# Kernel tuning notes

Measured on AMD Instinct MI355X. Metric: run time of the kernel, lower is better.

Reference implementation:

```python
import jax, jax.numpy as jnp
import numpy as np

EPS_COS = 1e-8
EPS_NORM = 1e-12
LN_EPS = 1e-5
OT_REG = 0.05
OT_ITERS = 5

B, L, D_IN, D_H = 16, 512, 1024, 1024


def setup_inputs() -> dict:
    key = jax.random.key(0)
    ks = jax.random.split(key, 16)
    p = lambda k, shape: 0.02 * jax.random.normal(k, shape, dtype=jnp.float32)
    return {
        "origin_seq": jax.random.normal(ks[0], (B, L, D_IN), dtype=jnp.float32),
        "target_seq": jax.random.normal(ks[1], (B, L, D_IN), dtype=jnp.float32),
        "W_ori": p(ks[2], (D_IN, D_H)), "b_ori": jnp.zeros((D_H,), jnp.float32),
        "W_tar": p(ks[3], (D_IN, D_H)), "b_tar": jnp.zeros((D_H,), jnp.float32),
        "W_ft": p(ks[4], (D_H, D_H)), "b_ft": jnp.zeros((D_H,), jnp.float32),
        "W_fo": p(ks[5], (D_H, D_H)), "b_fo": jnp.zeros((D_H,), jnp.float32),
        "W_fot": p(ks[6], (D_H, D_H)), "b_fot": jnp.zeros((D_H,), jnp.float32),
        "ln_g": jnp.ones((D_H,), jnp.float32), "ln_b": jnp.zeros((D_H,), jnp.float32),
    }


def _l2norm(x, eps):
    return x / jnp.maximum(jnp.linalg.norm(x, axis=-1, keepdims=True), eps)


def _forward(origin_seq, target_seq, W_ori, b_ori, W_tar, b_tar, W_ft, b_ft,
             W_fo, b_fo, W_fot, b_fot, ln_g, ln_b):
    ori = origin_seq @ W_ori + b_ori            # [B, Lo, H]
    tar = target_seq @ W_tar + b_tar            # [B, Lt, H]
    tar = tar @ W_ft + b_ft
    ori_fc = ori @ W_fo + b_fo
    ori_tp = ori @ W_fot + b_fot
    # cosine similarity cost: [B, Lt, Lo]
    C = jnp.einsum('bth,boh->bto', _l2norm(tar, EPS_COS), _l2norm(ori_fc, EPS_COS))
    # Sinkhorn: alternating row/col normalization of exp(C/eps)
    Q = jnp.exp(C / OT_REG)
    for _ in range(OT_ITERS):
        Q = Q / jnp.sum(Q, axis=-1, keepdims=True)
        Q = Q / jnp.sum(Q, axis=-2, keepdims=True)
    plan = _l2norm(Q, EPS_NORM)                 # F.normalize(dim=-1); dropout is eval no-op
    out = jnp.einsum('bto,boh->bth', plan, ori_tp) + tar
    mu = jnp.mean(out, axis=-1, keepdims=True)
    var = jnp.mean((out - mu) ** 2, axis=-1, keepdims=True)
    return ((out - mu) * jax.lax.rsqrt(var + LN_EPS)) * ln_g + ln_b


def reference(origin_seq, target_seq, W_ori, b_ori, W_tar, b_tar, W_ft, b_ft,
              W_fo, b_fo, W_fot, b_fot, ln_g, ln_b):
    return _forward(origin_seq, target_seq, W_ori, b_ori, W_tar, b_tar, W_ft, b_ft,
                    W_fo, b_fo, W_fot, b_fot, ln_g, ln_b)
```

## Files before the change

### kernel.cpp

```cpp
#include <hip/hip_runtime.h>
#include <hip/hip_bf16.h>
#include <math.h>

constexpr int Bn = 16;
constexpr int Ln = 512;
constexpr int Hn = 1024;
constexpr int RowsT = Bn * Ln;

typedef __attribute__((ext_vector_type(8))) short bf16x8;
typedef __attribute__((ext_vector_type(4))) float f32x4;
typedef __attribute__((ext_vector_type(8))) unsigned short u16x8;

__device__ __forceinline__ unsigned short f2bf(float f) {
  unsigned u = __float_as_uint(f);
  u += 0x7FFFu + ((u >> 16) & 1u);
  return (unsigned short)(u >> 16);
}
__device__ __forceinline__ float bf2f(unsigned short u) {
  return __uint_as_float(((unsigned)u) << 16);
}

__device__ __forceinline__ void gload_lds16(const void* g, void* l) {
  __builtin_amdgcn_global_load_lds(
      (const __attribute__((address_space(1))) void*)g,
      (__attribute__((address_space(3))) void*)l, 16, 0, 0);
}

__device__ __forceinline__ float block_reduce_sum(float v) {
  __shared__ float sbuf[8];
  const int lane = threadIdx.x & 63;
  const int wid = threadIdx.x >> 6;
#pragma unroll
  for (int off = 32; off > 0; off >>= 1) v += __shfl_down(v, off, 64);
  __syncthreads();
  if (lane == 0) sbuf[wid] = v;
  __syncthreads();
  if (threadIdx.x == 0) {
    float t = 0.f;
    const int nw = (blockDim.x + 63) >> 6;
    for (int i = 0; i < nw; ++i) t += sbuf[i];
    sbuf[0] = t;
  }
  __syncthreads();
  return sbuf[0];
}

__global__ __launch_bounds__(256) void conv_z(
    const float* __restrict__ s0, const float* __restrict__ s1,
    unsigned short* __restrict__ d0, unsigned short* __restrict__ d1) {
  const float* in = blockIdx.z ? s1 : s0;
  unsigned short* out = blockIdx.z ? d1 : d0;
  const size_t i = ((size_t)blockIdx.x * blockDim.x + threadIdx.x) * 8;
  const float4 a = *(const float4*)(in + i);
  const float4 b = *(const float4*)(in + i + 4);
  u16x8 r;
  r[0] = f2bf(a.x); r[1] = f2bf(a.y); r[2] = f2bf(a.z); r[3] = f2bf(a.w);
  r[4] = f2bf(b.x); r[5] = f2bf(b.y); r[6] = f2bf(b.z); r[7] = f2bf(b.w);
  *(u16x8*)(out + i) = r;
}

__global__ __launch_bounds__(256) void transpose_w3(
    const float* __restrict__ s0, const float* __restrict__ s1, const float* __restrict__ s2,
    unsigned short* __restrict__ d0, unsigned short* __restrict__ d1,
    unsigned short* __restrict__ d2, int K, int N) {
  const int z = blockIdx.z;
  const float* W = z == 0 ? s0 : (z == 1 ? s1 : s2);
  unsigned short* Wt = z == 0 ? d0 : (z == 1 ? d1 : d2);
  __shared__ float t[32][33];
  const int n0 = blockIdx.x * 32;
  const int k0 = blockIdx.y * 32;
  const int tx = threadIdx.x & 31;
  const int ty = threadIdx.x >> 5;
#pragma unroll
  for (int i = 0; i < 32; i += 8)
    t[ty + i][tx] = W[(size_t)(k0 + ty + i) * N + n0 + tx];
  __syncthreads();
#pragma unroll
  for (int i = 0; i < 32; i += 8)
    Wt[(size_t)(n0 + ty + i) * K + k0 + tx] = f2bf(t[tx][ty + i]);
}

__global__ __launch_bounds__(256) void bias_combine(
    const float* __restrict__ b1a, const float* __restrict__ Wa, const float* __restrict__ b2a,
    const float* __restrict__ b1b, const float* __restrict__ Wb, const float* __restrict__ b2b,
    const float* __restrict__ b1c, const float* __restrict__ Wc, const float* __restrict__ b2c,
    float* __restrict__ o0, float* __restrict__ o1, float* __restrict__ o2) {
  const int z = blockIdx.y;
  const float* b1 = z == 0 ? b1a : (z == 1 ? b1b : b1c);
  const float* W  = z == 0 ? Wa  : (z == 1 ? Wb  : Wc);
  const float* b2 = z == 0 ? b2a : (z == 1 ? b2b : b2c);
  float* out      = z == 0 ? o0  : (z == 1 ? o1  : o2);
  const int n = blockIdx.x * 256 + threadIdx.x;
  float s = b2[n];
  for (int j = 0; j < Hn; ++j) s += b1[j] * W[(size_t)j * Hn + n];
  out[n] = s;
}

#define MFMA_PROLOG(Aptr, Bptr, Kdim)                                          \
  constexpr int BK = 32;                                                       \
  __shared__ unsigned short As[128][BK];                                       \
  __shared__ unsigned short Bs[128][BK];                                       \
  const int tid = threadIdx.x;                                                 \
  const int wid = tid >> 6;                                                    \
  const int lane = tid & 63;                                                   \
  const int wr = (wid >> 1) * 64;                                              \
  const int wc = (wid & 1) * 64;                                               \
  const int sr = lane >> 2;                                                    \
  const int sk = (lane & 3) * 8;                                               \
  const size_t arow = (size_t)(row0 + wid * 32 + sr) * Kdim + sk;              \
  const size_t brow = (size_t)(col0 + wid * 32 + sr) * Kdim + sk;              \
  f32x4 acc[4][4] = {};                                                        \
  for (int k0 = 0; k0 < Kdim; k0 += BK) {                                      \
    gload_lds16(Aptr + arow + k0,                      &As[wid * 32][0]);      \
    gload_lds16(Aptr + arow + (size_t)16 * Kdim + k0,  &As[wid * 32 + 16][0]); \
    gload_lds16(Bptr + brow + k0,                      &Bs[wid * 32][0]);      \
    gload_lds16(Bptr + brow + (size_t)16 * Kdim + k0,  &Bs[wid * 32 + 16][0]); \
    __syncthreads();                                                           \
    bf16x8 af[4], bfr[4];                                                      \
    _Pragma("unroll")                                                          \
    for (int m = 0; m < 4; ++m)                                                \
      af[m] = *(const bf16x8*)&As[wr + m * 16 + (lane & 15)][(lane >> 4) * 8]; \
    _Pragma("unroll")                                                          \
    for (int n = 0; n < 4; ++n)                                                \
      bfr[n] = *(const bf16x8*)&Bs[wc + n * 16 + (lane & 15)][(lane >> 4) * 8];\
    _Pragma("unroll")                                                          \
    for (int m = 0; m < 4; ++m)                                                \
      _Pragma("unroll")                                                        \
      for (int n = 0; n < 4; ++n)                                              \
        acc[m][n] = __builtin_amdgcn_mfma_f32_16x16x32_bf16(af[m], bfr[n],     \
                                                            acc[m][n], 0, 0, 0);\
    __syncthreads();                                                           \
  }                                                                            \
  const int cr = (lane >> 4) * 4;                                              \
  const int cc = lane & 15;

__global__ __launch_bounds__(256) void mfma_gemm_w3(
    const unsigned short* __restrict__ A0, const unsigned short* __restrict__ A1,
    const unsigned short* __restrict__ A2,
    const unsigned short* __restrict__ B0, const unsigned short* __restrict__ B1,
    const unsigned short* __restrict__ B2,
    unsigned short* __restrict__ D0, unsigned short* __restrict__ D1,
    unsigned short* __restrict__ D2, int N, int K) {
  const int z = blockIdx.z;
  const unsigned short* A = z == 0 ? A0 : (z == 1 ? A1 : A2);
  const unsigned short* Bt = z == 0 ? B0 : (z == 1 ? B1 : B2);
  unsigned short* D = z == 0 ? D0 : (z == 1 ? D1 : D2);
  const int row0 = blockIdx.y * 128;
  const int col0 = blockIdx.x * 128;
  MFMA_PROLOG(A, Bt, K)
#pragma unroll
  for (int m = 0; m < 4; ++m) {
#pragma unroll
    for (int n = 0; n < 4; ++n) {
      const int gc = col0 + wc + n * 16 + cc;
#pragma unroll
      for (int r = 0; r < 4; ++r) {
        const int gr = row0 + wr + m * 16 + cr + r;
        D[(size_t)gr * N + gc] = f2bf(acc[m][n][r]);
      }
    }
  }
}

__global__ __launch_bounds__(256) void mfma_gemm_big(
    const unsigned short* __restrict__ Tb, const unsigned short* __restrict__ Ob,
    const unsigned short* __restrict__ W1, const unsigned short* __restrict__ W2,
    const unsigned short* __restrict__ W3,
    const float* __restrict__ bc1, const float* __restrict__ bc2,
    const float* __restrict__ bc3,
    unsigned short* __restrict__ Dtar, unsigned short* __restrict__ Dfc,
    unsigned short* __restrict__ DtpT) {
  const int id = blockIdx.x;
  const int xcd = id & 7;
  const int j = id >> 3;
  const int x = j & 7;
  const int rest = j >> 3;
  const int y = xcd + ((rest & 7) << 3);
  const int z = rest >> 3;
  const unsigned short* A = z == 0 ? Tb : Ob;
  const unsigned short* Bt = z == 0 ? W1 : (z == 1 ? W2 : W3);
  const float* bias = z == 0 ? bc1 : (z == 1 ? bc2 : bc3);
  const int row0 = y * 128;
  const int col0 = x * 128;
  MFMA_PROLOG(A, Bt, Hn)
  if (z != 2) {
    unsigned short* D = z == 0 ? Dtar : Dfc;
#pragma unroll
    for (int m = 0; m < 4; ++m) {
#pragma unroll
      for (int n = 0; n < 4; ++n) {
        const int gc = col0 + wc + n * 16 + cc;
        const float bv = bias[gc];
#pragma unroll
        for (int r = 0; r < 4; ++r) {
          const int gr = row0 + wr + m * 16 + cr + r;
          D[(size_t)gr * Hn + gc] = f2bf(acc[m][n][r] + bv);
        }
      }
    }
  } else {
#pragma unroll
    for (int m = 0; m < 4; ++m) {
      const int gr0 = row0 + wr + m * 16 + cr;
      const int b = gr0 >> 9;
      const int o = gr0 & 511;
#pragma unroll
      for (int n = 0; n < 4; ++n) {
        const int gc = col0 + wc + n * 16 + cc;
        const float bv = bias[gc];
        ushort4 w;
        w.x = f2bf(acc[m][n][0] + bv);
        w.y = f2bf(acc[m][n][1] + bv);
        w.z = f2bf(acc[m][n][2] + bv);
        w.w = f2bf(acc[m][n][3] + bv);
        *(ushort4*)(DtpT + ((size_t)b * Hn + gc) * Ln + o) = w;
      }
    }
  }
}

__global__ __launch_bounds__(256) void mfma_cos_exp(
    const unsigned short* __restrict__ TarBf, const unsigned short* __restrict__ FcBf,
    const float* __restrict__ rt, const float* __restrict__ rf,
    float* __restrict__ Q) {
  const int b = blockIdx.z;
  const unsigned short* Ab = TarBf + (size_t)b * Ln * Hn;
  const unsigned short* Bb = FcBf + (size_t)b * Ln * Hn;
  float* Qb = Q + (size_t)b * Ln * Ln;
  const int row0 = blockIdx.y * 128;
  const int col0 = blockIdx.x * 128;
  MFMA_PROLOG(Ab, Bb, Hn)
#pragma unroll
  for (int m = 0; m < 4; ++m) {
#pragma unroll
    for (int n = 0; n < 4; ++n) {
      const int o = col0 + wc + n * 16 + cc;
      const float rfo = rf[b * Ln + o] * 20.0f;
#pragma unroll
      for (int r = 0; r < 4; ++r) {
        const int t = row0 + wr + m * 16 + cr + r;
        const float c = acc[m][n][r] * rt[b * Ln + t] * rfo;
        Qb[(size_t)t * Ln + o] = __expf(c);
      }
    }
  }
}

__global__ __launch_bounds__(256) void mfma_out(
    const unsigned short* __restrict__ Plan, const unsigned short* __restrict__ TpT,
    const unsigned short* __restrict__ TarBf, float* __restrict__ Out) {
  const int b = blockIdx.z;
  const unsigned short* Ab = Plan + (size_t)b * Ln * Ln;
  const unsigned short* Bb = TpT + (size_t)b * Hn * Ln;
  const int row0 = blockIdx.y * 128;
  const int col0 = blockIdx.x * 128;
  MFMA_PROLOG(Ab, Bb, Ln)
#pragma unroll
  for (int m = 0; m < 4; ++m) {
#pragma unroll
    for (int n = 0; n < 4; ++n) {
      const int h = col0 + wc + n * 16 + cc;
#pragma unroll
      for (int r = 0; r < 4; ++r) {
        const int t = row0 + wr + m * 16 + cr + r;
        const size_t off = ((size_t)b * Ln + t) * Hn + h;
        Out[off] = acc[m][n][r] + bf2f(TarBf[off]);
      }
    }
  }
}

__global__ __launch_bounds__(256) void rownorm_z(
    const unsigned short* __restrict__ X0, const unsigned short* __restrict__ X1,
    float* __restrict__ r0, float* __restrict__ r1, float eps) {
  const unsigned short* X = blockIdx.y ? X1 : X0;
  float* r = blockIdx.y ? r1 : r0;
  const unsigned short* row = X + (size_t)blockIdx.x * Hn;
  const int i = threadIdx.x * 4;
  ushort4 v = *(const ushort4*)(row + i);
  float a0 = bf2f(v.x), a1 = bf2f(v.y), a2 = bf2f(v.z), a3 = bf2f(v.w);
  float s = block_reduce_sum(a0 * a0 + a1 * a1 + a2 * a2 + a3 * a3);
  if (threadIdx.x == 0) r[blockIdx.x] = 1.0f / fmaxf(sqrtf(s), eps);
}

__global__ __launch_bounds__(1024) void sinkhorn_fused(
    const float* __restrict__ Q, unsigned short* __restrict__ P) {
  const int b = blockIdx.x;
  const float* Qb = Q + (size_t)b * Ln * Ln;
  __shared__ __align__(16) float vsh[Ln];
  __shared__ __align__(16) float ush[Ln];
  __shared__ float part[1024];
  const int tid = threadIdx.x;
  const int wv = tid >> 6;
  const int lane = tid & 63;
  const int o = tid & 511;
  const int half = tid >> 9;
  if (tid < Ln) vsh[tid] = 1.0f;
  __syncthreads();
  for (int it = 0; it < 5; ++it) {
    for (int r = wv; r < Ln; r += 16) {
      const float* q = Qb + (size_t)r * Ln;
      const float4 a = *(const float4*)(q + lane * 8);
      const float4 c = *(const float4*)(q + lane * 8 + 4);
      const float4 va = *(const float4*)(vsh + lane * 8);
      const float4 vc = *(const float4*)(vsh + lane * 8 + 4);
      float s = a.x * va.x + a.y * va.y + a.z * va.z + a.w * va.w +
                c.x * vc.x + c.y * vc.y + c.z * vc.z + c.w * vc.w;
#pragma unroll
      for (int off = 32; off > 0; off >>= 1) s += __shfl_down(s, off, 64);
      if (lane == 0) ush[r] = 1.0f / s;
    }
    __syncthreads();
    float s = 0.f;
    const int t0 = half * 256;
#pragma unroll 4
    for (int t = t0; t < t0 + 256; ++t) s += Qb[(size_t)t * Ln + o] * ush[t];
    part[tid] = s;
    __syncthreads();
    if (tid < Ln) vsh[tid] = 1.0f / (part[tid] + part[tid + 512]);
    __syncthreads();
  }
  for (int r = wv; r < Ln; r += 16) {
    const float* q = Qb + (size_t)r * Ln;
    const float4 a = *(const float4*)(q + lane * 8);
    const float4 c = *(const float4*)(q + lane * 8 + 4);
    const float4 va = *(const float4*)(vsh + lane * 8);
    const float4 vc = *(const float4*)(vsh + lane * 8 + 4);
    float p[8];
    p[0] = a.x * va.x; p[1] = a.y * va.y; p[2] = a.z * va.z; p[3] = a.w * va.w;
    p[4] = c.x * vc.x; p[5] = c.y * vc.y; p[6] = c.z * vc.z; p[7] = c.w * vc.w;
    float s = 0.f;
#pragma unroll
    for (int k = 0; k < 8; ++k) s += p[k] * p[k];
#pragma unroll
    for (int off = 32; off > 0; off >>= 1) s += __shfl_down(s, off, 64);
    s = __shfl(s, 0, 64);
    const float rn = 1.0f / fmaxf(sqrtf(s), 1e-12f);
    u16x8 w;
#pragma unroll
    for (int k = 0; k < 8; ++k) w[k] = f2bf(p[k] * rn);
    *(u16x8*)(P + ((size_t)b * Ln + r) * Ln + lane * 8) = w;
  }
}

__global__ __launch_bounds__(256) void ln_kernel(
    float* __restrict__ Out, const float* __restrict__ g, const float* __restrict__ b) {
  float* row = Out + (size_t)blockIdx.x * Hn;
  const int tid = threadIdx.x;
  float4 v = reinterpret_cast<float4*>(row)[tid];
  float s = v.x + v.y + v.z + v.w;
  float ss = v.x * v.x + v.y * v.y + v.z * v.z + v.w * v.w;
  const float tot = block_reduce_sum(s);
  const float tot2 = block_reduce_sum(ss);
  const float mu = tot * (1.0f / Hn);
  const float var = tot2 * (1.0f / Hn) - mu * mu;
  const float rs = rsqrtf(var + 1e-5f);
  const float4 gg = reinterpret_cast<const float4*>(g)[tid];
  const float4 bb = reinterpret_cast<const float4*>(b)[tid];
  v.x = (v.x - mu) * rs * gg.x + bb.x;
  v.y = (v.y - mu) * rs * gg.y + bb.y;
  v.z = (v.z - mu) * rs * gg.z + bb.z;
  v.w = (v.w - mu) * rs * gg.w + bb.w;
  reinterpret_cast<float4*>(row)[tid] = v;
}

extern "C" void kernel_launch(void* const* d_in, const int* in_sizes, int n_in,
                              void* d_out, int out_size, void* d_ws, size_t ws_size,
                              hipStream_t stream) {
  const float* origin = (const float*)d_in[0];
  const float* target = (const float*)d_in[1];
  const float* W_ori = (const float*)d_in[2];
  const float* b_ori = (const float*)d_in[3];
  const float* W_tar = (const float*)d_in[4];
  const float* b_tar = (const float*)d_in[5];
  const float* W_ft = (const float*)d_in[6];
  const float* b_ft = (const float*)d_in[7];
  const float* W_fo = (const float*)d_in[8];
  const float* b_fo = (const float*)d_in[9];
  const float* W_fot = (const float*)d_in[10];
  const float* b_fot = (const float*)d_in[11];
  const float* ln_g = (const float*)d_in[12];
  const float* ln_b = (const float*)d_in[13];
  float* out = (float*)d_out;

  char* ws = (char*)d_ws;
  const size_t MB = 1048576;
  unsigned short* O_bf = (unsigned short*)(ws + 0);
  float* Qw = (float*)(ws + 0);
  unsigned short* T_bf = (unsigned short*)(ws + 16 * MB);
  unsigned short* plan_bf = (unsigned short*)(ws + 16 * MB);
  unsigned short* tar_bf = (unsigned short*)(ws + 32 * MB);
  unsigned short* fc_bf = (unsigned short*)(ws + 48 * MB);
  unsigned short* tpT = (unsigned short*)(ws + 64 * MB);
  unsigned short* Wc1T = (unsigned short*)(ws + 80 * MB);
  unsigned short* Wc2T = (unsigned short*)(ws + 82 * MB);
  unsigned short* Wc3T = (unsigned short*)(ws + 84 * MB);
  unsigned short* Wtar_bf = (unsigned short*)(ws + 86 * MB);
  unsigned short* Wori_bf = (unsigned short*)(ws + 88 * MB);
  unsigned short* WftT = (unsigned short*)(ws + 90 * MB);
  unsigned short* WfoT = (unsigned short*)(ws + 92 * MB);
  unsigned short* WfotT = (unsigned short*)(ws + 94 * MB);
  float* bc1 = (float*)(ws + 96 * MB);
  float* bc2 = bc1 + 1024;
  float* bc3 = bc2 + 1024;
  float* rt = bc3 + 1024;
  float* rf = rt + RowsT;

  const dim3 blk(256);

  conv_z<<<dim3(RowsT * Hn / 2048, 1, 2), blk, 0, stream>>>(origin, target, O_bf, T_bf);
  conv_z<<<dim3(Hn * Hn / 2048, 1, 2), blk, 0, stream>>>(W_tar, W_ori, Wtar_bf, Wori_bf);
  transpose_w3<<<dim3(32, 32, 3), blk, 0, stream>>>(W_ft, W_fo, W_fot,
                                                    WftT, WfoT, WfotT, Hn, Hn);
  bias_combine<<<dim3(4, 3), blk, 0, stream>>>(b_tar, W_ft, b_ft, b_ori, W_fo, b_fo,
                                               b_ori, W_fot, b_fot, bc1, bc2, bc3);
  mfma_gemm_w3<<<dim3(8, 8, 3), blk, 0, stream>>>(WftT, WfoT, WfotT,
                                                  Wtar_bf, Wori_bf, Wori_bf,
                                                  Wc1T, Wc2T, Wc3T, Hn, Hn);
  mfma_gemm_big<<<dim3(1536), blk, 0, stream>>>(T_bf, O_bf, Wc1T, Wc2T, Wc3T,
                                                bc1, bc2, bc3, tar_bf, fc_bf, tpT);
  rownorm_z<<<dim3(RowsT, 2), blk, 0, stream>>>(tar_bf, fc_bf, rt, rf, 1e-8f);
  mfma_cos_exp<<<dim3(4, 4, Bn), blk, 0, stream>>>(tar_bf, fc_bf, rt, rf, Qw);
  sinkhorn_fused<<<dim3(Bn), dim3(1024), 0, stream>>>(Qw, plan_bf);
  mfma_out<<<dim3(Hn / 128, Ln / 128, Bn), blk, 0, stream>>>(plan_bf, tpT, tar_bf, out);
  ln_kernel<<<dim3(RowsT), blk, 0, stream>>>(out, ln_g, ln_b);
}
```

Measured before the change: 479.6 us.

## Split Sinkhorn into grid-wide u/v step kernels and remap GEMM blocks across XCDs

The single-block-per-batch Sinkhorn kernel, which ran only 16 workgroups, is replaced by separate u_step, v_step and plan_prep kernels that spread the row and column reductions over many blocks. Each step now reads the 16 MB Q matrix from global memory or L2, and the chain adds 11 launches. The cos_exp and output GEMMs also switch to a 1D grid with XCD-aware block remapping, so that tiles of the same batch land on the same XCD and share its L2.

```diff
diff --git a/kernel.cpp b/kernel.cpp
--- a/kernel.cpp
+++ b/kernel.cpp
@@ -223,12 +223,18 @@
     const unsigned short* __restrict__ TarBf, const unsigned short* __restrict__ FcBf,
     const float* __restrict__ rt, const float* __restrict__ rf,
     float* __restrict__ Q) {
-  const int b = blockIdx.z;
+  const int id = blockIdx.x;
+  const int xcd = id & 7;
+  const int r2 = id >> 3;
+  const int x = r2 & 3;
+  const int yb = xcd + ((r2 >> 2) << 3);
+  const int y = yb & 3;
+  const int b = yb >> 2;
   const unsigned short* Ab = TarBf + (size_t)b * Ln * Hn;
   const unsigned short* Bb = FcBf + (size_t)b * Ln * Hn;
   float* Qb = Q + (size_t)b * Ln * Ln;
-  const int row0 = blockIdx.y * 128;
-  const int col0 = blockIdx.x * 128;
+  const int row0 = y * 128;
+  const int col0 = x * 128;
   MFMA_PROLOG(Ab, Bb, Hn)
 #pragma unroll
   for (int m = 0; m < 4; ++m) {
@@ -249,11 +255,17 @@
 __global__ __launch_bounds__(256) void mfma_out(
     const unsigned short* __restrict__ Plan, const unsigned short* __restrict__ TpT,
     const unsigned short* __restrict__ TarBf, float* __restrict__ Out) {
-  const int b = blockIdx.z;
+  const int id = blockIdx.x;
+  const int xcd = id & 7;
+  const int r2 = id >> 3;
+  const int x = r2 & 7;
+  const int yb = xcd + ((r2 >> 3) << 3);
+  const int y = yb & 3;
+  const int b = yb >> 2;
   const unsigned short* Ab = Plan + (size_t)b * Ln * Ln;
   const unsigned short* Bb = TpT + (size_t)b * Hn * Ln;
-  const int row0 = blockIdx.y * 128;
-  const int col0 = blockIdx.x * 128;
+  const int row0 = y * 128;
+  const int col0 = x * 128;
   MFMA_PROLOG(Ab, Bb, Ln)
 #pragma unroll
   for (int m = 0; m < 4; ++m) {
@@ -283,64 +295,70 @@
   if (threadIdx.x == 0) r[blockIdx.x] = 1.0f / fmaxf(sqrtf(s), eps);
 }
 
-__global__ __launch_bounds__(1024) void sinkhorn_fused(
-    const float* __restrict__ Q, unsigned short* __restrict__ P) {
-  const int b = blockIdx.x;
+template<bool FIRST>
+__global__ __launch_bounds__(256) void u_step(
+    const float* __restrict__ Q, const float* __restrict__ v, float* __restrict__ u) {
+  const int row = blockIdx.x * 4 + (threadIdx.x >> 6);
+  const int b = row >> 9;
+  const int lane = threadIdx.x & 63;
+  const float* q = Q + (size_t)row * Ln;
+  const float4 a = *(const float4*)(q + lane * 8);
+  const float4 c = *(const float4*)(q + lane * 8 + 4);
+  float s;
+  if (FIRST) {
+    s = a.x + a.y + a.z + a.w + c.x + c.y + c.z + c.w;
+  } else {
+    const float* vb = v + b * Ln;
+    const float4 va = *(const float4*)(vb + lane * 8);
+    const float4 vc = *(const float4*)(vb + lane * 8 + 4);
+    s = a.x * va.x + a.y * va.y + a.z * va.z + a.w * va.w +
+        c.x * vc.x + c.y * vc.y + c.z * vc.z + c.w * vc.w;
+  }
+#pragma unroll
+  for (int off = 32; off > 0; off >>= 1) s += __shfl_down(s, off, 64);
+  if (lane == 0) u[row] = 1.0f / s;
+}
+
+__global__ __launch_bounds__(256) void v_step(
+    const float* __restrict__ Q, const float* __restrict__ u, float* __restrict__ v) {
+  const int b = blockIdx.y;
   const float* Qb = Q + (size_t)b * Ln * Ln;
-  __shared__ __align__(16) float vsh[Ln];
-  __shared__ __align__(16) float ush[Ln];
-  __shared__ float part[1024];
+  __shared__ float us[Ln];
+  __shared__ float part[4][64];
   const int tid = threadIdx.x;
-  const int wv = tid >> 6;
-  const int lane = tid & 63;
-  const int o = tid & 511;
-  const int half = tid >> 9;
-  if (tid < Ln) vsh[tid] = 1.0f;
-  __syncthreads();
-  for (int it = 0; it < 5; ++it) {
-    for (int r = wv; r < Ln; r += 16) {
-      const float* q = Qb + (size_t)r * Ln;
-      const float4 a = *(const float4*)(q + lane * 8);
-      const float4 c = *(const float4*)(q + lane * 8 + 4);
-      const float4 va = *(const float4*)(vsh + lane * 8);
-      const float4 vc = *(const float4*)(vsh + lane * 8 + 4);
-      float s = a.x * va.x + a.y * va.y + a.z * va.z + a.w * va.w +
-                c.x * vc.x + c.y * vc.y + c.z * vc.z + c.w * vc.w;
-#pragma unroll
-      for (int off = 32; off > 0; off >>= 1) s += __shfl_down(s, off, 64);
-      if (lane == 0) ush[r] = 1.0f / s;
-    }
-    __syncthreads();
-    float s = 0.f;
-    const int t0 = half * 256;
+  us[tid] = u[b * Ln + tid];
+  us[tid + 256] = u[b * Ln + tid + 256];
+  __syncthreads();
+  const int c = tid & 63;
+  const int chunk = tid >> 6;
+  const int o = blockIdx.x * 64 + c;
+  float s = 0.f;
 #pragma unroll 4
-    for (int t = t0; t < t0 + 256; ++t) s += Qb[(size_t)t * Ln + o] * ush[t];
-    part[tid] = s;
-    __syncthreads();
-    if (tid < Ln) vsh[tid] = 1.0f / (part[tid] + part[tid + 512]);
-    __syncthreads();
-  }
-  for (int r = wv; r < Ln; r += 16) {
-    const float* q = Qb + (size_t)r * Ln;
-    const float4 a = *(const float4*)(q + lane * 8);
-    const float4 c = *(const float4*)(q + lane * 8 + 4);
-    const float4 va = *(const float4*)(vsh + lane * 8);
-    const float4 vc = *(const float4*)(vsh + lane * 8 + 4);
-    float p[8];
-    p[0] = a.x * va.x; p[1] = a.y * va.y; p[2] = a.z * va.z; p[3] = a.w * va.w;
-    p[4] = c.x * vc.x; p[5] = c.y * vc.y; p[6] = c.z * vc.z; p[7] = c.w * vc.w;
-    float s = 0.f;
-#pragma unroll
-    for (int k = 0; k < 8; ++k) s += p[k] * p[k];
-#pragma unroll
-    for (int off = 32; off > 0; off >>= 1) s += __shfl_down(s, off, 64);
-    s = __shfl(s, 0, 64);
-    const float rn = 1.0f / fmaxf(sqrtf(s), 1e-12f);
-    u16x8 w;
-#pragma unroll
-    for (int k = 0; k < 8; ++k) w[k] = f2bf(p[k] * rn);
-    *(u16x8*)(P + ((size_t)b * Ln + r) * Ln + lane * 8) = w;
-  }
+  for (int t = chunk * 128; t < chunk * 128 + 128; ++t)
+    s += Qb[(size_t)t * Ln + o] * us[t];
+  part[chunk][c] = s;
+  __syncthreads();
+  if (chunk == 0)
+    v[b * Ln + o] = 1.0f / (part[0][c] + part[1][c] + part[2][c] + part[3][c]);
+}
+
+__global__ __launch_bounds__(256) void plan_prep(
+    const float* __restrict__ Q, const float* __restrict__ v,
+    unsigned short* __restrict__ P) {
+  const int row = blockIdx.x;
+  const int b = row >> 9;
+  const float* q = Q + (size_t)row * Ln;
+  const float* vb = v + b * Ln;
+  const int i = threadIdx.x * 2;
+  const float2 qq = *(const float2*)(q + i);
+  const float2 vv = *(const float2*)(vb + i);
+  const float p0 = qq.x * vv.x, p1 = qq.y * vv.y;
+  const float s = block_reduce_sum(p0 * p0 + p1 * p1);
+  const float rn = 1.0f / fmaxf(sqrtf(s), 1e-12f);
+  ushort2 w;
+  w.x = f2bf(p0 * rn);
+  w.y = f2bf(p1 * rn);
+  *(ushort2*)(P + (size_t)row * Ln + i) = w;
 }
 
 __global__ __launch_bounds__(256) void ln_kernel(
@@ -405,6 +423,8 @@
   float* bc3 = bc2 + 1024;
   float* rt = bc3 + 1024;
   float* rf = rt + RowsT;
+  float* uu = rf + RowsT;
+  float* vv = uu + RowsT;
 
   const dim3 blk(256);
 
@@ -420,8 +440,14 @@
   mfma_gemm_big<<<dim3(1536), blk, 0, stream>>>(T_bf, O_bf, Wc1T, Wc2T, Wc3T,
                                                 bc1, bc2, bc3, tar_bf, fc_bf, tpT);
   rownorm_z<<<dim3(RowsT, 2), blk, 0, stream>>>(tar_bf, fc_bf, rt, rf, 1e-8f);
-  mfma_cos_exp<<<dim3(4, 4, Bn), blk, 0, stream>>>(tar_bf, fc_bf, rt, rf, Qw);
-  sinkhorn_fused<<<dim3(Bn), dim3(1024), 0, stream>>>(Qw, plan_bf);
-  mfma_out<<<dim3(Hn / 128, Ln / 128, Bn), blk, 0, stream>>>(plan_bf, tpT, tar_bf, out);
+  mfma_cos_exp<<<dim3(256), blk, 0, stream>>>(tar_bf, fc_bf, rt, rf, Qw);
+  u_step<true><<<dim3(RowsT / 4), blk, 0, stream>>>(Qw, vv, uu);
+  v_step<<<dim3(Ln / 64, Bn), blk, 0, stream>>>(Qw, uu, vv);
+  for (int it = 1; it < 5; ++it) {
+    u_step<false><<<dim3(RowsT / 4), blk, 0, stream>>>(Qw, vv, uu);
+    v_step<<<dim3(Ln / 64, Bn), blk, 0, stream>>>(Qw, uu, vv);
+  }
+  plan_prep<<<dim3(RowsT), blk, 0, stream>>>(Qw, vv, plan_bf);
+  mfma_out<<<dim3(512), blk, 0, stream>>>(plan_bf, tpT, tar_bf, out);
   ln_kernel<<<dim3(RowsT), blk, 0, stream>>>(out, ln_g, ln_b);
 }
```

Result: faster. 426.7 us (-11.0%).
